# Optimization experiments

Measured on AMD Instinct MI355X. Metric: run time of the kernel, lower is better.

The kernel has to match this reference:

```python
import jax, jax.numpy as jnp
import numpy as np

N = 100000
E = 1600000
F_IN = 1433
HID = 64
HEADS = 2
CLS = 7


def setup_inputs() -> dict:
    key = jax.random.key(0)
    ks = jax.random.split(key, 12)
    x = jax.random.normal(ks[0], (N, F_IN), dtype=jnp.float32)
    edge_index = jax.random.randint(ks[1], (2, E), 0, N, dtype=jnp.int32)
    s1 = 1.0 / np.sqrt(F_IN)
    s2 = 1.0 / np.sqrt(HID)
    W1 = jax.random.uniform(ks[2], (F_IN, HID), jnp.float32, -s1, s1)
    b1 = jnp.zeros((HID,), jnp.float32)
    W2 = jax.random.uniform(ks[3], (HID, HID), jnp.float32, -s2, s2)
    b2 = jnp.zeros((HID,), jnp.float32)
    Wg = jax.random.uniform(ks[4], (HID, HEADS * CLS), jnp.float32, -s2, s2)
    att_src = jax.random.normal(ks[5], (HEADS, CLS), jnp.float32) * 0.1
    att_dst = jax.random.normal(ks[6], (HEADS, CLS), jnp.float32) * 0.1
    bg = jnp.zeros((HEADS * CLS,), jnp.float32)
    return {"x": x, "edge_index": edge_index, "W1": W1, "b1": b1,
            "W2": W2, "b2": b2, "Wg": Wg, "att_src": att_src,
            "att_dst": att_dst, "bg": bg}


def _add_self_loops(edge_index, n):
    loop = jnp.arange(n, dtype=edge_index.dtype)
    src = jnp.concatenate([edge_index[0], loop])
    dst = jnp.concatenate([edge_index[1], loop])
    return src, dst


def _gcn_layer(x, W, b, src, dst, n):
    # symmetric normalization with self-loops (PyG GCNConv)
    deg = jax.ops.segment_sum(jnp.ones_like(src, dtype=x.dtype), dst, num_segments=n)
    dinv = jnp.where(deg > 0, jax.lax.rsqrt(deg), 0.0)
    norm = dinv[src] * dinv[dst]  # [E+N]
    h = x @ W  # transform before propagate (in >= out)
    msg = h[src] * norm[:, None]
    out = jax.ops.segment_sum(msg, dst, num_segments=n)
    return out + b


def _gat_layer(x, Wg, att_src, att_dst, bg, src, dst, n):
    h = (x @ Wg).reshape(n, HEADS, CLS)  # [N,H,C]
    a_src = jnp.sum(h * att_src, axis=-1)  # [N,H]
    a_dst = jnp.sum(h * att_dst, axis=-1)
    e = jax.nn.leaky_relu(a_src[src] + a_dst[dst], 0.2)  # [E+N,H]
    m = jax.ops.segment_max(e, dst, num_segments=n)  # [N,H]
    m = jnp.where(jnp.isfinite(m), m, 0.0)
    p = jnp.exp(e - m[dst])
    s = jax.ops.segment_sum(p, dst, num_segments=n)
    alpha = p / (s[dst] + 1e-16)  # segment softmax, [E+N,H]
    out = jax.ops.segment_sum(h[src] * alpha[:, :, None], dst, num_segments=n)
    return out.reshape(n, HEADS * CLS) + bg


def reference(x, edge_index, W1, b1, W2, b2, Wg, att_src, att_dst, bg):
    src, dst = _add_self_loops(edge_index, N)
    h = jax.nn.relu(_gcn_layer(x, W1, b1, src, dst, N))
    h = jax.nn.relu(_gcn_layer(h, W2, b2, src, dst, N))
    h = _gat_layer(h, Wg, att_src, att_dst, bg, src, dst, N)
    return jax.nn.log_softmax(h, axis=1)
```

## Files before the change

kernel.cpp:

```cpp
#include <hip/hip_runtime.h>
#include <hip/hip_bf16.h>

#define F_IN 1433
#define HID  64
#define C14  14

typedef __attribute__((ext_vector_type(8))) short short8;
typedef __attribute__((ext_vector_type(4))) float float4v;

__device__ inline short f2bf(float f) {
    union { float f; unsigned u; } c; c.f = f;
    unsigned u = c.u;
    u += 0x7fffu + ((u >> 16) & 1u);
    return (short)(u >> 16);
}

__device__ inline unsigned packbf(float a, float b) {
    union { float f; unsigned u; } x, y;
    x.f = a; y.f = b;
    unsigned ua = x.u; ua += 0x7fffu + ((ua >> 16) & 1u);
    unsigned ub = y.u; ub += 0x7fffu + ((ub >> 16) & 1u);
    return (ua >> 16) | (ub & 0xffff0000u);
}


__global__ void k_zero_int(int* __restrict__ p, int n) {
    int i = blockIdx.x * 256 + threadIdx.x;
    if (i < n) p[i] = 0;
}

__global__ void k_hist(const int* __restrict__ dst, int* __restrict__ cnt, int E) {
    int e = blockIdx.x * 256 + threadIdx.x;
    if (e < E) atomicAdd(&cnt[dst[e]], 1);
}

__global__ void k_dinv(const int* __restrict__ cnt, float* __restrict__ dinv, int n) {
    int i = blockIdx.x * 256 + threadIdx.x;
    if (i < n) dinv[i] = rsqrtf((float)cnt[i] + 1.0f);
}

__global__ __launch_bounds__(1024) void k_scan1(const int* __restrict__ cnt,
                                                int* __restrict__ excl,
                                                int* __restrict__ bsum, int n) {
    __shared__ int sd[1024];
    int tid = threadIdx.x;
    int g = blockIdx.x * 1024 + tid;
    int v = (g < n) ? cnt[g] : 0;
    sd[tid] = v;
    __syncthreads();
    for (int off = 1; off < 1024; off <<= 1) {
        int t = (tid >= off) ? sd[tid - off] : 0;
        __syncthreads();
        sd[tid] += t;
        __syncthreads();
    }
    if (g < n) excl[g] = sd[tid] - v;
    if (tid == 1023) bsum[blockIdx.x] = sd[1023];
}

__global__ __launch_bounds__(128) void k_scan2(const int* __restrict__ bsum,
                                               int* __restrict__ boff, int nb) {
    __shared__ int sd[128];
    int tid = threadIdx.x;
    int v = (tid < nb) ? bsum[tid] : 0;
    sd[tid] = v;
    __syncthreads();
    for (int off = 1; off < 128; off <<= 1) {
        int t = (tid >= off) ? sd[tid - off] : 0;
        __syncthreads();
        sd[tid] += t;
        __syncthreads();
    }
    if (tid < nb) boff[tid] = sd[tid] - v;
}

__global__ __launch_bounds__(1024) void k_scan3(int* __restrict__ rowst,
                                                const int* __restrict__ boff,
                                                int* __restrict__ fill, int n, int E) {
    int tid = threadIdx.x;
    int g = blockIdx.x * 1024 + tid;
    if (g < n) {
        int v = rowst[g] + boff[blockIdx.x];
        rowst[g] = v;
        fill[g] = v;
    }
    if (g == 0) rowst[n] = E;
}

__global__ void k_scatter(const int* __restrict__ ei, int* __restrict__ fill,
                          int* __restrict__ esrc, int E) {
    int e = blockIdx.x * 256 + threadIdx.x;
    if (e < E) {
        int s = ei[e];
        int d = ei[E + e];
        int pos = atomicAdd(&fill[d], 1);
        esrc[pos] = s;
    }
}


__global__ void k_prep_bf(const float* __restrict__ W, short* __restrict__ Bf,
                          int K, int nchunk) {
    int id = blockIdx.x * 256 + threadIdx.x;
    int total = nchunk * 512;
    if (id >= total) return;
    int l = id & 63;
    int s = (id >> 6) & 1;
    int t = (id >> 7) & 3;
    int ks = id >> 9;
    int n = t * 16 + (l & 15);
    int k0 = ks * 64 + s * 32 + (l >> 4) * 8;
    short tmp[8];
#pragma unroll
    for (int j = 0; j < 8; j++) {
        int k = k0 + j;
        tmp[j] = (k < K) ? f2bf(W[(size_t)k * 64 + n]) : (short)0;
    }
    *(short8*)&Bf[(size_t)id * 8] = *(const short8*)tmp;
}


__global__ __launch_bounds__(256) void gemm_mfma(const float* __restrict__ A, int K, int nchunk,
                                                 int M, const short* __restrict__ Bf,
                                                 const float* __restrict__ dinv,
                                                 float* __restrict__ C) {
    __shared__ short As[128 * 64];
    __shared__ short Bs[4096];
    const int tid = threadIdx.x;
    const int w = tid >> 6, l = tid & 63;
    const int row0 = blockIdx.x * 128;
    const int m16 = l & 15, q = l >> 4;

    const int lrow = tid >> 5;
    const int lcol = (tid & 31) * 2;
    const bool interior = (row0 + 128 <= M);
    const size_t rs = (size_t)K;
    const float* __restrict__ Abase = A + (size_t)min(row0 + lrow, M - 1) * rs + lcol;

    float4v acc[2][4];
#pragma unroll
    for (int mi = 0; mi < 2; mi++)
#pragma unroll
        for (int t = 0; t < 4; t++) acc[mi][t] = (float4v){0.f, 0.f, 0.f, 0.f};

    float pre[32];
    int4 preB0, preB1;

    auto issue = [&](int ks) {
        const int kb = ks * 64;
        if (interior && (kb + 64 <= K)) {
#pragma unroll
            for (int it = 0; it < 16; it++) {
                const float* p2 = Abase + kb + (size_t)(it * 8) * rs;
                pre[2 * it]     = p2[0];
                pre[2 * it + 1] = p2[1];
            }
        } else {
#pragma unroll
            for (int it = 0; it < 16; it++) {
                int row = min(row0 + it * 8 + lrow, M - 1);
                int c = kb + lcol;
                const float* p2 = A + (size_t)row * rs + c;
                pre[2 * it]     = (c < K)     ? p2[0] : 0.f;
                pre[2 * it + 1] = (c + 1 < K) ? p2[1] : 0.f;
            }
        }
        const short* bsrc = Bf + (size_t)ks * 4096;
        preB0 = *(const int4*)&bsrc[tid * 16];
        preB1 = *(const int4*)&bsrc[tid * 16 + 8];
    };

    auto stage = [&]() {
        char* As8 = (char*)As;
#pragma unroll
        for (int it = 0; it < 16; it++) {
            int row = it * 8 + lrow;
            unsigned u = packbf(pre[2 * it], pre[2 * it + 1]);
            int p = lcol >> 3;
            int pp = p ^ (row & 7);
            *(unsigned*)&As8[row * 128 + pp * 16 + (lcol & 7) * 2] = u;
        }
        *(int4*)&Bs[tid * 16] = preB0;
        *(int4*)&Bs[tid * 16 + 8] = preB1;
    };

    auto compute = [&]() {
#pragma unroll
        for (int s = 0; s < 2; s++) {
            short8 a[2];
#pragma unroll
            for (int mi = 0; mi < 2; mi++) {
                int row = w * 32 + mi * 16 + m16;
                int p = s * 4 + q;
                a[mi] = *(const short8*)&As[row * 64 + (p ^ (row & 7)) * 8];
            }
#pragma unroll
            for (int t = 0; t < 4; t++) {
                short8 b = *(const short8*)&Bs[(t * 2 + s) * 512 + l * 8];
                acc[0][t] = __builtin_amdgcn_mfma_f32_16x16x32_bf16(a[0], b, acc[0][t], 0, 0, 0);
                acc[1][t] = __builtin_amdgcn_mfma_f32_16x16x32_bf16(a[1], b, acc[1][t], 0, 0, 0);
            }
        }
    };

    issue(0);
    stage();
    __syncthreads();
    for (int ks = 0; ks < nchunk; ks++) {
        bool more = (ks + 1 < nchunk);
        if (more) issue(ks + 1);
        compute();
        __syncthreads();
        if (more) {
            stage();
            __syncthreads();
        }
    }

#pragma unroll
    for (int mi = 0; mi < 2; mi++) {
#pragma unroll
        for (int i = 0; i < 4; i++) {
            int rr = row0 + w * 32 + mi * 16 + q * 4 + i;
            if (rr < M) {
                float dv = dinv ? dinv[rr] : 1.f;
#pragma unroll
                for (int t = 0; t < 4; t++)
                    C[(size_t)rr * 64 + t * 16 + m16] = acc[mi][t][i] * dv;
            }
        }
    }
}


__global__ __launch_bounds__(256) void gcn_prop(const float* __restrict__ H, float* __restrict__ O,
                                                const int* __restrict__ rowst,
                                                const int* __restrict__ esrc,
                                                const float* __restrict__ dinv,
                                                const float* __restrict__ bias, int n) {
    int i = blockIdx.x * 16 + (threadIdx.x >> 4);
    if (i >= n) return;
    int c0 = (threadIdx.x & 15) * 4;
    const float* __restrict__ Hc = H + c0;
    float4 acc = *(const float4*)&Hc[(size_t)i * 64];
    int j0 = rowst[i], j1 = rowst[i + 1];
    int j = j0;
    for (; j + 8 <= j1; j += 8) {
        int s0 = esrc[j], s1 = esrc[j + 1], s2 = esrc[j + 2], s3 = esrc[j + 3];
        int s4 = esrc[j + 4], s5 = esrc[j + 5], s6 = esrc[j + 6], s7 = esrc[j + 7];
        float4 h0 = *(const float4*)&Hc[(size_t)s0 * 64];
        float4 h1 = *(const float4*)&Hc[(size_t)s1 * 64];
        float4 h2 = *(const float4*)&Hc[(size_t)s2 * 64];
        float4 h3 = *(const float4*)&Hc[(size_t)s3 * 64];
        float4 h4 = *(const float4*)&Hc[(size_t)s4 * 64];
        float4 h5 = *(const float4*)&Hc[(size_t)s5 * 64];
        float4 h6 = *(const float4*)&Hc[(size_t)s6 * 64];
        float4 h7 = *(const float4*)&Hc[(size_t)s7 * 64];
        float tx = ((h0.x + h1.x) + (h2.x + h3.x)) + ((h4.x + h5.x) + (h6.x + h7.x));
        float ty = ((h0.y + h1.y) + (h2.y + h3.y)) + ((h4.y + h5.y) + (h6.y + h7.y));
        float tz = ((h0.z + h1.z) + (h2.z + h3.z)) + ((h4.z + h5.z) + (h6.z + h7.z));
        float tw = ((h0.w + h1.w) + (h2.w + h3.w)) + ((h4.w + h5.w) + (h6.w + h7.w));
        acc.x += tx; acc.y += ty; acc.z += tz; acc.w += tw;
    }
    if (j + 4 <= j1) {
        int s0 = esrc[j], s1 = esrc[j + 1], s2 = esrc[j + 2], s3 = esrc[j + 3];
        float4 h0 = *(const float4*)&Hc[(size_t)s0 * 64];
        float4 h1 = *(const float4*)&Hc[(size_t)s1 * 64];
        float4 h2 = *(const float4*)&Hc[(size_t)s2 * 64];
        float4 h3 = *(const float4*)&Hc[(size_t)s3 * 64];
        acc.x += (h0.x + h1.x) + (h2.x + h3.x);
        acc.y += (h0.y + h1.y) + (h2.y + h3.y);
        acc.z += (h0.z + h1.z) + (h2.z + h3.z);
        acc.w += (h0.w + h1.w) + (h2.w + h3.w);
        j += 4;
    }
    for (; j < j1; j++) {
        int s = esrc[j];
        float4 hv = *(const float4*)&Hc[(size_t)s * 64];
        acc.x += hv.x; acc.y += hv.y; acc.z += hv.z; acc.w += hv.w;
    }
    float di = dinv[i];
    float4 b4 = *(const float4*)&bias[c0];
    float4 o;
    o.x = fmaxf(acc.x * di + b4.x, 0.f);
    o.y = fmaxf(acc.y * di + b4.y, 0.f);
    o.z = fmaxf(acc.z * di + b4.z, 0.f);
    o.w = fmaxf(acc.w * di + b4.w, 0.f);
    *(float4*)&O[(size_t)i * 64 + c0] = o;
}


__global__ __launch_bounds__(256) void gat_gemm(const float* __restrict__ X,
                                                const float* __restrict__ Wg,
                                                const float* __restrict__ att_src,
                                                const float* __restrict__ att_dst,
                                                float* __restrict__ HG,
                                                float* __restrict__ AS, float* __restrict__ AD,
                                                int n) {
    __shared__ float xs[64 * 65];
    __shared__ float wg[64 * C14];
    __shared__ float hgs[64 * 15];
    const int tid = threadIdx.x;
    const int n0 = blockIdx.x * 64;

    for (int i = tid; i < 64 * C14; i += 256) wg[i] = Wg[i];
    for (int i = tid * 4; i < 4096; i += 1024) {
        int nn = i >> 6, k = i & 63;
        int g = n0 + nn;
        float4 v = make_float4(0.f, 0.f, 0.f, 0.f);
        if (g < n) v = *(const float4*)&X[(size_t)g * 64 + k];
        xs[nn * 65 + k] = v.x;
        xs[nn * 65 + k + 1] = v.y;
        xs[nn * 65 + k + 2] = v.z;
        xs[nn * 65 + k + 3] = v.w;
    }
    __syncthreads();

    const int nn = tid & 63;
    const int qq = tid >> 6;
    float acc[4] = {0.f, 0.f, 0.f, 0.f};
    for (int k = 0; k < 64; k++) {
        float a = xs[nn * 65 + k];
#pragma unroll
        for (int j = 0; j < 4; j++) {
            int c = qq + 4 * j;
            if (c < C14) acc[j] += a * wg[k * C14 + c];
        }
    }
    int g = n0 + nn;
#pragma unroll
    for (int j = 0; j < 4; j++) {
        int c = qq + 4 * j;
        if (c < C14) {
            hgs[nn * 15 + c] = acc[j];
            if (g < n) HG[(size_t)g * 16 + c] = acc[j];
        }
    }
    __syncthreads();

    if (tid < 128) {
        int nloc = tid & 63;
        int h = tid >> 6;
        int gg = n0 + nloc;
        if (gg < n) {
            float s1 = 0.f, s2 = 0.f;
#pragma unroll
            for (int cc = 0; cc < 7; cc++) {
                float hv = hgs[nloc * 15 + h * 7 + cc];
                s1 += hv * att_src[h * 7 + cc];
                s2 += hv * att_dst[h * 7 + cc];
            }
            AS[(size_t)gg * 2 + h] = s1;
            AD[(size_t)gg * 2 + h] = s2;
        }
    }
}


__global__ __launch_bounds__(256) void gat_agg(const float* __restrict__ HG,
                                               const float* __restrict__ AS,
                                               const float* __restrict__ AD,
                                               const int* __restrict__ rowst,
                                               const int* __restrict__ esrc,
                                               const float* __restrict__ bg,
                                               float* __restrict__ out, int n) {
    int i = blockIdx.x * 16 + (threadIdx.x >> 4);
    if (i >= n) return;
    int c = threadIdx.x & 15;
    int h = (c < 7) ? 0 : 1;
    float adst = AD[(size_t)i * 2 + h];
    float asrc = AS[(size_t)i * 2 + h];
    auto lrelu = [](float x) { return x > 0.f ? x : 0.2f * x; };

    float m = lrelu(asrc + adst);
    float ssum = 1.f;
    float acc = (c < C14) ? HG[(size_t)i * 16 + c] : 0.f;

    int j0 = rowst[i], j1 = rowst[i + 1];
    int j = j0;
    for (; j + 8 <= j1; j += 8) {
        int s[8];
#pragma unroll
        for (int u = 0; u < 8; u++) s[u] = esrc[j + u];
        float e[8], g[8];
#pragma unroll
        for (int u = 0; u < 8; u++) {
            e[u] = lrelu(AS[(size_t)s[u] * 2 + h] + adst);
            g[u] = (c < C14) ? HG[(size_t)s[u] * 16 + c] : 0.f;
        }
        float em = fmaxf(fmaxf(fmaxf(e[0], e[1]), fmaxf(e[2], e[3])),
                         fmaxf(fmaxf(e[4], e[5]), fmaxf(e[6], e[7])));
        float nm = fmaxf(m, em);
        float sc = __expf(m - nm);
        float p[8];
#pragma unroll
        for (int u = 0; u < 8; u++) p[u] = __expf(e[u] - nm);
        float ps = ((p[0] + p[1]) + (p[2] + p[3])) + ((p[4] + p[5]) + (p[6] + p[7]));
        float gs = ((g[0] * p[0] + g[1] * p[1]) + (g[2] * p[2] + g[3] * p[3]))
                 + ((g[4] * p[4] + g[5] * p[5]) + (g[6] * p[6] + g[7] * p[7]));
        ssum = ssum * sc + ps;
        acc = acc * sc + gs;
        m = nm;
    }
    if (j + 4 <= j1) {
        int s[4];
#pragma unroll
        for (int u = 0; u < 4; u++) s[u] = esrc[j + u];
        float e[4], g[4];
#pragma unroll
        for (int u = 0; u < 4; u++) {
            e[u] = lrelu(AS[(size_t)s[u] * 2 + h] + adst);
            g[u] = (c < C14) ? HG[(size_t)s[u] * 16 + c] : 0.f;
        }
        float em = fmaxf(fmaxf(e[0], e[1]), fmaxf(e[2], e[3]));
        float nm = fmaxf(m, em);
        float sc = __expf(m - nm);
        float p[4];
#pragma unroll
        for (int u = 0; u < 4; u++) p[u] = __expf(e[u] - nm);
        float ps = (p[0] + p[1]) + (p[2] + p[3]);
        float gs = (g[0] * p[0] + g[1] * p[1]) + (g[2] * p[2] + g[3] * p[3]);
        ssum = ssum * sc + ps;
        acc = acc * sc + gs;
        m = nm;
        j += 4;
    }
    for (; j < j1; j++) {
        int s = esrc[j];
        float e = lrelu(AS[(size_t)s * 2 + h] + adst);
        float gv = (c < C14) ? HG[(size_t)s * 16 + c] : 0.f;
        float nm = fmaxf(m, e);
        float sc = __expf(m - nm);
        float pe = __expf(e - nm);
        ssum = ssum * sc + pe;
        acc = acc * sc + gv * pe;
        m = nm;
    }

    float v = acc / ssum + ((c < C14) ? bg[c] : 0.f);

    float vv = (c < C14) ? v : -__builtin_inff();
    float maxv = vv;
#pragma unroll
    for (int d = 1; d < 16; d <<= 1) maxv = fmaxf(maxv, __shfl_xor(maxv, d, 16));
    float ee = (c < C14) ? __expf(v - maxv) : 0.f;
    float s2 = ee;
#pragma unroll
    for (int d = 1; d < 16; d <<= 1) s2 += __shfl_xor(s2, d, 16);
    if (c < C14) out[(size_t)i * C14 + c] = v - maxv - __logf(s2);
}


extern "C" void kernel_launch(void* const* d_in, const int* in_sizes, int n_in,
                              void* d_out, int out_size, void* d_ws, size_t ws_size,
                              hipStream_t stream) {
    const float* x       = (const float*)d_in[0];
    const int*   ei      = (const int*)d_in[1];
    const float* W1      = (const float*)d_in[2];
    const float* b1      = (const float*)d_in[3];
    const float* W2      = (const float*)d_in[4];
    const float* b2      = (const float*)d_in[5];
    const float* Wg      = (const float*)d_in[6];
    const float* att_src = (const float*)d_in[7];
    const float* att_dst = (const float*)d_in[8];
    const float* bg      = (const float*)d_in[9];

    const int N = in_sizes[0] / F_IN;
    const int E = in_sizes[1] / 2;
    const int NC1 = (F_IN + 63) / 64;
    const int NC2 = 1;

    char* p = (char*)d_ws;
    auto alloc = [&](size_t bytes) {
        char* r = p;
        p += (bytes + 255) & ~(size_t)255;
        return r;
    };
    float* h    = (float*)alloc((size_t)N * 64 * 4);
    float* g    = (float*)alloc((size_t)N * 64 * 4);
    float* hg   = (float*)alloc((size_t)N * 16 * 4);
    float* As   = (float*)alloc((size_t)N * 2 * 4);
    float* Ad   = (float*)alloc((size_t)N * 2 * 4);
    float* dinv = (float*)alloc((size_t)N * 4);
    int* cnt    = (int*)alloc((size_t)N * 4);
    int* rowst  = (int*)alloc((size_t)(N + 1) * 4);
    int* fill   = (int*)alloc((size_t)N * 4);
    int* esrc   = (int*)alloc((size_t)E * 4);
    int* bsum   = (int*)alloc(128 * 4);
    int* boff   = (int*)alloc(128 * 4);
    short* Bf1  = (short*)alloc((size_t)NC1 * 4096 * 2);
    short* Bf2  = (short*)alloc((size_t)NC2 * 4096 * 2);

    const int gN = (N + 255) / 256;
    const int gE = (E + 255) / 256;
    const int nb = (N + 1023) / 1024;
    const int g16 = (N + 15) / 16;
    const int gT64 = (N + 63) / 64;
    const int gT128 = (N + 127) / 128;

    k_prep_bf<<<(NC1 * 512 + 255) / 256, 256, 0, stream>>>(W1, Bf1, F_IN, NC1);
    k_prep_bf<<<(NC2 * 512 + 255) / 256, 256, 0, stream>>>(W2, Bf2, 64, NC2);

    k_zero_int<<<gN, 256, 0, stream>>>(cnt, N);
    k_hist<<<gE, 256, 0, stream>>>(ei + E, cnt, E);
    k_dinv<<<gN, 256, 0, stream>>>(cnt, dinv, N);
    k_scan1<<<nb, 1024, 0, stream>>>(cnt, rowst, bsum, N);
    k_scan2<<<1, 128, 0, stream>>>(bsum, boff, nb);
    k_scan3<<<nb, 1024, 0, stream>>>(rowst, boff, fill, N, E);
    k_scatter<<<gE, 256, 0, stream>>>(ei, fill, esrc, E);

    gemm_mfma<<<gT128, 256, 0, stream>>>(x, F_IN, NC1, N, Bf1, dinv, h);
    gcn_prop<<<g16, 256, 0, stream>>>(h, g, rowst, esrc, dinv, b1, N);
    gemm_mfma<<<gT128, 256, 0, stream>>>(g, 64, NC2, N, Bf2, dinv, h);
    gcn_prop<<<g16, 256, 0, stream>>>(h, g, rowst, esrc, dinv, b2, N);
    gat_gemm<<<gT64, 256, 0, stream>>>(g, Wg, att_src, att_dst, hg, As, Ad, N);
    gat_agg<<<g16, 256, 0, stream>>>(hg, As, Ad, rowst, esrc, bg, (float*)d_out, N);
}
```

Measured before the change: 1.196 ms.

## Store GCN hidden features in bf16, pack GAT src scores into HG, fuse setup kernels

The GEMM epilogue now writes the transformed features as packed bf16 pairs, so each gcn_prop gather moves half the bytes per neighbor. It also packs the per-node GAT source attention scores into the two unused padding slots of the 16-wide HG rows. gat_agg then fetches them with a lane shuffle instead of a separate gather. The weight-prep and count-zeroing kernels are merged into one setup kernel, and the dinv computation moves into the first scan kernel, cutting launches. The cost is bf16 rounding of intermediate features, which adds numerical error to the propagated sums.

```diff
diff --git a/kernel.cpp b/kernel.cpp
--- a/kernel.cpp
+++ b/kernel.cpp
@@ -23,29 +23,54 @@
     return (ua >> 16) | (ub & 0xffff0000u);
 }
 
-
-__global__ void k_zero_int(int* __restrict__ p, int n) {
+__device__ inline float bflo(unsigned u) {
+    union { unsigned u; float f; } c; c.u = u << 16; return c.f;
+}
+__device__ inline float bfhi(unsigned u) {
+    union { unsigned u; float f; } c; c.u = u & 0xffff0000u; return c.f;
+}
+
+
+__global__ void k_setup(const float* __restrict__ W1, const float* __restrict__ W2,
+                        short* __restrict__ Bf1, short* __restrict__ Bf2,
+                        int* __restrict__ cnt, int n, int prep1, int prep2) {
     int i = blockIdx.x * 256 + threadIdx.x;
-    if (i < n) p[i] = 0;
-}
+    if (i < prep1 + prep2) {
+        const float* W; short* Bf; int K; int id;
+        if (i < prep1) { W = W1; Bf = Bf1; K = F_IN; id = i; }
+        else           { W = W2; Bf = Bf2; K = 64;   id = i - prep1; }
+        int l = id & 63;
+        int s = (id >> 6) & 1;
+        int t = (id >> 7) & 3;
+        int ks = id >> 9;
+        int nn = t * 16 + (l & 15);
+        int k0 = ks * 64 + s * 32 + (l >> 4) * 8;
+        short tmp[8];
+#pragma unroll
+        for (int j = 0; j < 8; j++) {
+            int k = k0 + j;
+            tmp[j] = (k < K) ? f2bf(W[(size_t)k * 64 + nn]) : (short)0;
+        }
+        *(short8*)&Bf[(size_t)id * 8] = *(const short8*)tmp;
+    }
+    if (i < n) cnt[i] = 0;
+}
+
 
 __global__ void k_hist(const int* __restrict__ dst, int* __restrict__ cnt, int E) {
     int e = blockIdx.x * 256 + threadIdx.x;
     if (e < E) atomicAdd(&cnt[dst[e]], 1);
 }
 
-__global__ void k_dinv(const int* __restrict__ cnt, float* __restrict__ dinv, int n) {
-    int i = blockIdx.x * 256 + threadIdx.x;
-    if (i < n) dinv[i] = rsqrtf((float)cnt[i] + 1.0f);
-}
-
 __global__ __launch_bounds__(1024) void k_scan1(const int* __restrict__ cnt,
                                                 int* __restrict__ excl,
-                                                int* __restrict__ bsum, int n) {
+                                                int* __restrict__ bsum,
+                                                float* __restrict__ dinv, int n) {
     __shared__ int sd[1024];
     int tid = threadIdx.x;
     int g = blockIdx.x * 1024 + tid;
     int v = (g < n) ? cnt[g] : 0;
+    if (g < n) dinv[g] = rsqrtf((float)v + 1.0f);
     sd[tid] = v;
     __syncthreads();
     for (int off = 1; off < 1024; off <<= 1) {
@@ -99,31 +124,10 @@
 }
 
 
-__global__ void k_prep_bf(const float* __restrict__ W, short* __restrict__ Bf,
-                          int K, int nchunk) {
-    int id = blockIdx.x * 256 + threadIdx.x;
-    int total = nchunk * 512;
-    if (id >= total) return;
-    int l = id & 63;
-    int s = (id >> 6) & 1;
-    int t = (id >> 7) & 3;
-    int ks = id >> 9;
-    int n = t * 16 + (l & 15);
-    int k0 = ks * 64 + s * 32 + (l >> 4) * 8;
-    short tmp[8];
-#pragma unroll
-    for (int j = 0; j < 8; j++) {
-        int k = k0 + j;
-        tmp[j] = (k < K) ? f2bf(W[(size_t)k * 64 + n]) : (short)0;
-    }
-    *(short8*)&Bf[(size_t)id * 8] = *(const short8*)tmp;
-}
-
-
 __global__ __launch_bounds__(256) void gemm_mfma(const float* __restrict__ A, int K, int nchunk,
                                                  int M, const short* __restrict__ Bf,
                                                  const float* __restrict__ dinv,
-                                                 float* __restrict__ C) {
+                                                 unsigned* __restrict__ C) {
     __shared__ short As[128 * 64];
     __shared__ short Bs[4096];
     const int tid = threadIdx.x;
@@ -224,69 +228,74 @@
             int rr = row0 + w * 32 + mi * 16 + q * 4 + i;
             if (rr < M) {
                 float dv = dinv ? dinv[rr] : 1.f;
-#pragma unroll
-                for (int t = 0; t < 4; t++)
-                    C[(size_t)rr * 64 + t * 16 + m16] = acc[mi][t][i] * dv;
+                uint2 uu;
+                uu.x = packbf(acc[0 + mi * 0][0][0], 0.f);
+                uu.x = packbf(acc[mi][0][i] * dv, acc[mi][1][i] * dv);
+                uu.y = packbf(acc[mi][2][i] * dv, acc[mi][3][i] * dv);
+                *(uint2*)&C[(size_t)rr * 32 + 2 * m16] = uu;
             }
         }
     }
 }
 
 
-__global__ __launch_bounds__(256) void gcn_prop(const float* __restrict__ H, float* __restrict__ O,
+__global__ __launch_bounds__(256) void gcn_prop(const uint2* __restrict__ Hb, float* __restrict__ O,
                                                 const int* __restrict__ rowst,
                                                 const int* __restrict__ esrc,
                                                 const float* __restrict__ dinv,
                                                 const float* __restrict__ bias, int n) {
     int i = blockIdx.x * 16 + (threadIdx.x >> 4);
     if (i >= n) return;
-    int c0 = (threadIdx.x & 15) * 4;
-    const float* __restrict__ Hc = H + c0;
-    float4 acc = *(const float4*)&Hc[(size_t)i * 64];
+    int L = threadIdx.x & 15;
+    const uint2* __restrict__ Hr = Hb + L;
+
+    uint2 sv = Hr[(size_t)i * 16];
+    float a0 = bflo(sv.x), a1 = bfhi(sv.x), a2 = bflo(sv.y), a3 = bfhi(sv.y);
+
     int j0 = rowst[i], j1 = rowst[i + 1];
     int j = j0;
     for (; j + 8 <= j1; j += 8) {
-        int s0 = esrc[j], s1 = esrc[j + 1], s2 = esrc[j + 2], s3 = esrc[j + 3];
-        int s4 = esrc[j + 4], s5 = esrc[j + 5], s6 = esrc[j + 6], s7 = esrc[j + 7];
-        float4 h0 = *(const float4*)&Hc[(size_t)s0 * 64];
-        float4 h1 = *(const float4*)&Hc[(size_t)s1 * 64];
-        float4 h2 = *(const float4*)&Hc[(size_t)s2 * 64];
-        float4 h3 = *(const float4*)&Hc[(size_t)s3 * 64];
-        float4 h4 = *(const float4*)&Hc[(size_t)s4 * 64];
-        float4 h5 = *(const float4*)&Hc[(size_t)s5 * 64];
-        float4 h6 = *(const float4*)&Hc[(size_t)s6 * 64];
-        float4 h7 = *(const float4*)&Hc[(size_t)s7 * 64];
-        float tx = ((h0.x + h1.x) + (h2.x + h3.x)) + ((h4.x + h5.x) + (h6.x + h7.x));
-        float ty = ((h0.y + h1.y) + (h2.y + h3.y)) + ((h4.y + h5.y) + (h6.y + h7.y));
-        float tz = ((h0.z + h1.z) + (h2.z + h3.z)) + ((h4.z + h5.z) + (h6.z + h7.z));
-        float tw = ((h0.w + h1.w) + (h2.w + h3.w)) + ((h4.w + h5.w) + (h6.w + h7.w));
-        acc.x += tx; acc.y += ty; acc.z += tz; acc.w += tw;
+        int s[8];
+#pragma unroll
+        for (int u = 0; u < 8; u++) s[u] = esrc[j + u];
+        uint2 v[8];
+#pragma unroll
+        for (int u = 0; u < 8; u++) v[u] = Hr[(size_t)s[u] * 16];
+        float t0 = ((bflo(v[0].x) + bflo(v[1].x)) + (bflo(v[2].x) + bflo(v[3].x)))
+                 + ((bflo(v[4].x) + bflo(v[5].x)) + (bflo(v[6].x) + bflo(v[7].x)));
+        float t1 = ((bfhi(v[0].x) + bfhi(v[1].x)) + (bfhi(v[2].x) + bfhi(v[3].x)))
+                 + ((bfhi(v[4].x) + bfhi(v[5].x)) + (bfhi(v[6].x) + bfhi(v[7].x)));
+        float t2 = ((bflo(v[0].y) + bflo(v[1].y)) + (bflo(v[2].y) + bflo(v[3].y)))
+                 + ((bflo(v[4].y) + bflo(v[5].y)) + (bflo(v[6].y) + bflo(v[7].y)));
+        float t3 = ((bfhi(v[0].y) + bfhi(v[1].y)) + (bfhi(v[2].y) + bfhi(v[3].y)))
+                 + ((bfhi(v[4].y) + bfhi(v[5].y)) + (bfhi(v[6].y) + bfhi(v[7].y)));
+        a0 += t0; a1 += t1; a2 += t2; a3 += t3;
     }
     if (j + 4 <= j1) {
-        int s0 = esrc[j], s1 = esrc[j + 1], s2 = esrc[j + 2], s3 = esrc[j + 3];
-        float4 h0 = *(const float4*)&Hc[(size_t)s0 * 64];
-        float4 h1 = *(const float4*)&Hc[(size_t)s1 * 64];
-        float4 h2 = *(const float4*)&Hc[(size_t)s2 * 64];
-        float4 h3 = *(const float4*)&Hc[(size_t)s3 * 64];
-        acc.x += (h0.x + h1.x) + (h2.x + h3.x);
-        acc.y += (h0.y + h1.y) + (h2.y + h3.y);
-        acc.z += (h0.z + h1.z) + (h2.z + h3.z);
-        acc.w += (h0.w + h1.w) + (h2.w + h3.w);
+        int s[4];
+#pragma unroll
+        for (int u = 0; u < 4; u++) s[u] = esrc[j + u];
+        uint2 v[4];
+#pragma unroll
+        for (int u = 0; u < 4; u++) v[u] = Hr[(size_t)s[u] * 16];
+        a0 += (bflo(v[0].x) + bflo(v[1].x)) + (bflo(v[2].x) + bflo(v[3].x));
+        a1 += (bfhi(v[0].x) + bfhi(v[1].x)) + (bfhi(v[2].x) + bfhi(v[3].x));
+        a2 += (bflo(v[0].y) + bflo(v[1].y)) + (bflo(v[2].y) + bflo(v[3].y));
+        a3 += (bfhi(v[0].y) + bfhi(v[1].y)) + (bfhi(v[2].y) + bfhi(v[3].y));
         j += 4;
     }
     for (; j < j1; j++) {
-        int s = esrc[j];
-        float4 hv = *(const float4*)&Hc[(size_t)s * 64];
-        acc.x += hv.x; acc.y += hv.y; acc.z += hv.z; acc.w += hv.w;
-    }
+        uint2 v = Hr[(size_t)esrc[j] * 16];
+        a0 += bflo(v.x); a1 += bfhi(v.x); a2 += bflo(v.y); a3 += bfhi(v.y);
+    }
+
     float di = dinv[i];
-    float4 b4 = *(const float4*)&bias[c0];
-    float4 o;
-    o.x = fmaxf(acc.x * di + b4.x, 0.f);
-    o.y = fmaxf(acc.y * di + b4.y, 0.f);
-    o.z = fmaxf(acc.z * di + b4.z, 0.f);
-    o.w = fmaxf(acc.w * di + b4.w, 0.f);
-    *(float4*)&O[(size_t)i * 64 + c0] = o;
+    float o0 = fmaxf(a0 * di + bias[L],      0.f);
+    float o1 = fmaxf(a1 * di + bias[L + 16], 0.f);
+    float o2 = fmaxf(a2 * di + bias[L + 32], 0.f);
+    float o3 = fmaxf(a3 * di + bias[L + 48], 0.f);
+    float* Or = O + (size_t)i * 64;
+    Or[L] = o0; Or[L + 16] = o1; Or[L + 32] = o2; Or[L + 48] = o3;
 }
 
 
@@ -295,7 +304,7 @@
                                                 const float* __restrict__ att_src,
                                                 const float* __restrict__ att_dst,
                                                 float* __restrict__ HG,
-                                                float* __restrict__ AS, float* __restrict__ AD,
+                                                float* __restrict__ AD,
                                                 int n) {
     __shared__ float xs[64 * 65];
     __shared__ float wg[64 * C14];
@@ -350,7 +359,7 @@
                 s1 += hv * att_src[h * 7 + cc];
                 s2 += hv * att_dst[h * 7 + cc];
             }
-            AS[(size_t)gg * 2 + h] = s1;
+            HG[(size_t)gg * 16 + 14 + h] = s1;
             AD[(size_t)gg * 2 + h] = s2;
         }
     }
@@ -358,7 +367,6 @@
 
 
 __global__ __launch_bounds__(256) void gat_agg(const float* __restrict__ HG,
-                                               const float* __restrict__ AS,
                                                const float* __restrict__ AD,
                                                const int* __restrict__ rowst,
                                                const int* __restrict__ esrc,
@@ -368,13 +376,15 @@
     if (i >= n) return;
     int c = threadIdx.x & 15;
     int h = (c < 7) ? 0 : 1;
+    int asl = 14 + h;
     float adst = AD[(size_t)i * 2 + h];
-    float asrc = AS[(size_t)i * 2 + h];
     auto lrelu = [](float x) { return x > 0.f ? x : 0.2f * x; };
 
+    float gself = HG[(size_t)i * 16 + c];
+    float asrc = __shfl(gself, asl, 16);
     float m = lrelu(asrc + adst);
     float ssum = 1.f;
-    float acc = (c < C14) ? HG[(size_t)i * 16 + c] : 0.f;
+    float acc = (c < C14) ? gself : 0.f;
 
     int j0 = rowst[i], j1 = rowst[i + 1];
     int j = j0;
@@ -382,11 +392,13 @@
         int s[8];
 #pragma unroll
         for (int u = 0; u < 8; u++) s[u] = esrc[j + u];
-        float e[8], g[8];
+        float gv[8], e[8];
+#pragma unroll
+        for (int u = 0; u < 8; u++) gv[u] = HG[(size_t)s[u] * 16 + c];
 #pragma unroll
         for (int u = 0; u < 8; u++) {
-            e[u] = lrelu(AS[(size_t)s[u] * 2 + h] + adst);
-            g[u] = (c < C14) ? HG[(size_t)s[u] * 16 + c] : 0.f;
+            e[u] = lrelu(__shfl(gv[u], asl, 16) + adst);
+            if (c >= C14) gv[u] = 0.f;
         }
         float em = fmaxf(fmaxf(fmaxf(e[0], e[1]), fmaxf(e[2], e[3])),
                          fmaxf(fmaxf(e[4], e[5]), fmaxf(e[6], e[7])));
@@ -396,8 +408,8 @@
 #pragma unroll
         for (int u = 0; u < 8; u++) p[u] = __expf(e[u] - nm);
         float ps = ((p[0] + p[1]) + (p[2] + p[3])) + ((p[4] + p[5]) + (p[6] + p[7]));
-        float gs = ((g[0] * p[0] + g[1] * p[1]) + (g[2] * p[2] + g[3] * p[3]))
-                 + ((g[4] * p[4] + g[5] * p[5]) + (g[6] * p[6] + g[7] * p[7]));
+        float gs = ((gv[0] * p[0] + gv[1] * p[1]) + (gv[2] * p[2] + gv[3] * p[3]))
+                 + ((gv[4] * p[4] + gv[5] * p[5]) + (gv[6] * p[6] + gv[7] * p[7]));
         ssum = ssum * sc + ps;
         acc = acc * sc + gs;
         m = nm;
@@ -406,11 +418,13 @@
         int s[4];
 #pragma unroll
         for (int u = 0; u < 4; u++) s[u] = esrc[j + u];
-        float e[4], g[4];
+        float gv[4], e[4];
+#pragma unroll
+        for (int u = 0; u < 4; u++) gv[u] = HG[(size_t)s[u] * 16 + c];
 #pragma unroll
         for (int u = 0; u < 4; u++) {
-            e[u] = lrelu(AS[(size_t)s[u] * 2 + h] + adst);
-            g[u] = (c < C14) ? HG[(size_t)s[u] * 16 + c] : 0.f;
+            e[u] = lrelu(__shfl(gv[u], asl, 16) + adst);
+            if (c >= C14) gv[u] = 0.f;
         }
         float em = fmaxf(fmaxf(e[0], e[1]), fmaxf(e[2], e[3]));
         float nm = fmaxf(m, em);
@@ -419,16 +433,16 @@
 #pragma unroll
         for (int u = 0; u < 4; u++) p[u] = __expf(e[u] - nm);
         float ps = (p[0] + p[1]) + (p[2] + p[3]);
-        float gs = (g[0] * p[0] + g[1] * p[1]) + (g[2] * p[2] + g[3] * p[3]);
+        float gs = (gv[0] * p[0] + gv[1] * p[1]) + (gv[2] * p[2] + gv[3] * p[3]);
         ssum = ssum * sc + ps;
         acc = acc * sc + gs;
         m = nm;
         j += 4;
     }
     for (; j < j1; j++) {
-        int s = esrc[j];
-        float e = lrelu(AS[(size_t)s * 2 + h] + adst);
-        float gv = (c < C14) ? HG[(size_t)s * 16 + c] : 0.f;
+        float gv = HG[(size_t)esrc[j] * 16 + c];
+        float e = lrelu(__shfl(gv, asl, 16) + adst);
+        if (c >= C14) gv = 0.f;
         float nm = fmaxf(m, e);
         float sc = __expf(m - nm);
         float pe = __expf(e - nm);
@@ -476,10 +490,9 @@
         p += (bytes + 255) & ~(size_t)255;
         return r;
     };
-    float* h    = (float*)alloc((size_t)N * 64 * 4);
+    unsigned* h = (unsigned*)alloc((size_t)N * 32 * 4);
     float* g    = (float*)alloc((size_t)N * 64 * 4);
     float* hg   = (float*)alloc((size_t)N * 16 * 4);
-    float* As   = (float*)alloc((size_t)N * 2 * 4);
     float* Ad   = (float*)alloc((size_t)N * 2 * 4);
     float* dinv = (float*)alloc((size_t)N * 4);
     int* cnt    = (int*)alloc((size_t)N * 4);
@@ -497,22 +510,20 @@
     const int g16 = (N + 15) / 16;
     const int gT64 = (N + 63) / 64;
     const int gT128 = (N + 127) / 128;
-
-    k_prep_bf<<<(NC1 * 512 + 255) / 256, 256, 0, stream>>>(W1, Bf1, F_IN, NC1);
-    k_prep_bf<<<(NC2 * 512 + 255) / 256, 256, 0, stream>>>(W2, Bf2, 64, NC2);
-
-    k_zero_int<<<gN, 256, 0, stream>>>(cnt, N);
+    const int prep1 = NC1 * 512, prep2 = NC2 * 512;
+
+    k_setup<<<gN, 256, 0, stream>>>(W1, W2, Bf1, Bf2, cnt, N, prep1, prep2);
+
     k_hist<<<gE, 256, 0, stream>>>(ei + E, cnt, E);
-    k_dinv<<<gN, 256, 0, stream>>>(cnt, dinv, N);
-    k_scan1<<<nb, 1024, 0, stream>>>(cnt, rowst, bsum, N);
+    k_scan1<<<nb, 1024, 0, stream>>>(cnt, rowst, bsum, dinv, N);
     k_scan2<<<1, 128, 0, stream>>>(bsum, boff, nb);
     k_scan3<<<nb, 1024, 0, stream>>>(rowst, boff, fill, N, E);
     k_scatter<<<gE, 256, 0, stream>>>(ei, fill, esrc, E);
 
     gemm_mfma<<<gT128, 256, 0, stream>>>(x, F_IN, NC1, N, Bf1, dinv, h);
-    gcn_prop<<<g16, 256, 0, stream>>>(h, g, rowst, esrc, dinv, b1, N);
+    gcn_prop<<<g16, 256, 0, stream>>>((const uint2*)h, g, rowst, esrc, dinv, b1, N);
     gemm_mfma<<<gT128, 256, 0, stream>>>(g, 64, NC2, N, Bf2, dinv, h);
-    gcn_prop<<<g16, 256, 0, stream>>>(h, g, rowst, esrc, dinv, b2, N);
-    gat_gemm<<<gT64, 256, 0, stream>>>(g, Wg, att_src, att_dst, hg, As, Ad, N);
-    gat_agg<<<g16, 256, 0, stream>>>(hg, As, Ad, rowst, esrc, bg, (float*)d_out, N);
-}
+    gcn_prop<<<g16, 256, 0, stream>>>((const uint2*)h, g, rowst, esrc, dinv, b2, N);
+    gat_gemm<<<gT64, 256, 0, stream>>>(g, Wg, att_src, att_dst, hg, Ad, N);
+    gat_agg<<<g16, 256, 0, stream>>>(hg, Ad, rowst, esrc, bg, (float*)d_out, N);
+}
```

Result: faster. 1.145 ms (-4.3%).
